# Performance work log

Hardware: AMD Instinct MI355X
Metric: run time of the kernel (lower is better)

Reference implementation:

```python
import jax, jax.numpy as jnp
import numpy as np

N, F, E, T = 50000, 128, 800000, 8


def setup_inputs() -> dict:
    key = jax.random.key(0)
    ks = jax.random.split(key, 10)
    s = 1.0 / np.sqrt(F)
    return {
        "x": jax.random.normal(ks[0], (N, F), jnp.float32),
        "edge_index": jax.random.randint(ks[1], (2, E), 0, N, jnp.int64),
        "edge_weight": jax.random.uniform(ks[2], (E,), jnp.float32),
        "W0": jax.random.normal(ks[3], (F, F), jnp.float32) * s,
        "Wih": jax.random.normal(ks[4], (3 * F, F), jnp.float32) * s,
        "Whh": jax.random.normal(ks[5], (3 * F, F), jnp.float32) * s,
        "bih": jax.random.normal(ks[6], (3 * F,), jnp.float32) * s,
        "bhh": jax.random.normal(ks[7], (3 * F,), jnp.float32) * s,
        "Wlin": jax.random.normal(ks[8], (T, F), jnp.float32) * s,
        "blin": jax.random.normal(ks[9], (T,), jnp.float32) * s,
    }


def _evolve_weight(W0, Wih, Whh, bih, bhh):
    # One GRU step with input = hidden = W0 (rows of weight matrix as batch).
    gi = W0 @ Wih.T + bih  # [F, 3F]
    gh = W0 @ Whh.T + bhh
    ir, iz, inn = jnp.split(gi, 3, axis=1)
    hr, hz, hn = jnp.split(gh, 3, axis=1)
    r = jax.nn.sigmoid(ir + hr)
    z = jax.nn.sigmoid(iz + hz)
    n = jnp.tanh(inn + r * hn)
    return (1.0 - z) * n + z * W0  # [F, F]


def reference(x, edge_index, edge_weight, W0, Wih, Whh, bih, bhh, Wlin, blin):
    n_nodes = x.shape[0]
    W = _evolve_weight(W0, Wih, Whh, bih, bhh)
    # gcn_norm with added self-loops (fill value 1.0), symmetric normalization
    loop = jnp.arange(n_nodes, dtype=edge_index.dtype)
    row = jnp.concatenate([edge_index[0], loop])
    col = jnp.concatenate([edge_index[1], loop])
    ew = jnp.concatenate([edge_weight, jnp.ones((n_nodes,), edge_weight.dtype)])
    deg = jax.ops.segment_sum(ew, col, num_segments=n_nodes)
    dinv = jnp.where(deg > 0, jax.lax.rsqrt(jnp.where(deg > 0, deg, 1.0)), 0.0)
    norm = dinv[row] * ew * dinv[col]  # [E+N]
    xw = x @ W  # [N, F]
    h = jax.ops.segment_sum(norm[:, None] * xw[row], col, num_segments=n_nodes)
    h = jax.nn.relu(h)
    return h @ Wlin.T + blin  # [N, n_target]
```

## Files before the change

kernel.cpp:

```cpp
#include <hip/hip_runtime.h>
#include <math.h>

#define F 128
#define FIX18     262144.0f
#define INV18     (1.0f / 262144.0f)
#define EVB 256

using bf16x8 = __attribute__((ext_vector_type(8))) short;
using f32x4  = __attribute__((ext_vector_type(4))) float;

__device__ inline int read_idx(const int* ei, long long elem, int i64) {
    return i64 ? (int)((const long long*)ei)[elem] : ei[elem];
}
__device__ inline unsigned int f2bf_rn(float f) {
    unsigned int b = __float_as_uint(f);
    return (b + 0x7FFFu + ((b >> 16) & 1u)) >> 16;
}
__device__ inline float bflo(unsigned int u) { return __uint_as_float(u << 16); }
__device__ inline float bfhi(unsigned int u) { return __uint_as_float(u & 0xFFFF0000u); }

__device__ inline void acc8(float* acc, float wt, uint4 v) {
    acc[0] += wt * bflo(v.x); acc[1] += wt * bfhi(v.x);
    acc[2] += wt * bflo(v.y); acc[3] += wt * bfhi(v.y);
    acc[4] += wt * bflo(v.z); acc[5] += wt * bfhi(v.z);
    acc[6] += wt * bflo(v.w); acc[7] += wt * bfhi(v.w);
}

__device__ inline int detect_i64(const int* ei, int* sh) {
    if (threadIdx.x == 0) {
        int i64 = 1;
        for (int j = 0; j < 32; ++j) if (ei[2 * j + 1] != 0) { i64 = 0; break; }
        *sh = i64;
    }
    __syncthreads();
    return *sh;
}

__global__ __launch_bounds__(256) void k_count_evolve(
        const int* __restrict__ ei, const float* __restrict__ ew,
        unsigned int* __restrict__ packed8, int* __restrict__ pos,
        int E, int N,
        const float* __restrict__ W0, const float* __restrict__ Wih,
        const float* __restrict__ Whh, const float* __restrict__ bih,
        const float* __restrict__ bhh,
        unsigned short* __restrict__ Wth, unsigned short* __restrict__ Wtl) {
    __shared__ int i64sh;
    int wave = threadIdx.x >> 6, lane = threadIdx.x & 63;
    if ((int)blockIdx.x >= EVB) {
        int i64 = detect_i64(ei, &i64sh);
        int e = ((int)blockIdx.x - EVB) * 256 + threadIdx.x;
        if (e >= E) return;
        int c = read_idx(ei, (long long)E + e, i64);
        unsigned int copy = blockIdx.x & 7;
        unsigned int u = (1u << 24) | (unsigned int)(ew[e] * FIX18 + 0.5f);
        unsigned int old = atomicAdd(&packed8[(size_t)copy * N + c], u);
        pos[e] = (int)((old >> 24) | (copy << 24));
        return;
    }
    int gw = (int)blockIdx.x * 4 + wave;
    int pairBase = gw * 16;
    int i = pairBase >> 7;
    int jb = pairBase & 127;
    int lp = lane & 15, sl = lane >> 4;
    int j = jb + lp;
    const float* w0p = W0 + (size_t)i * F;
    const float* pir = Wih + (size_t)j * F;
    const float* piz = Wih + (size_t)(j + F) * F;
    const float* pin = Wih + (size_t)(j + 2 * F) * F;
    const float* phr = Whh + (size_t)j * F;
    const float* phz = Whh + (size_t)(j + F) * F;
    const float* phn = Whh + (size_t)(j + 2 * F) * F;
    float air = 0, aiz = 0, ain = 0, ahr = 0, ahz = 0, ahn = 0;
    int k0 = sl * 32;
    #pragma unroll
    for (int kk = 0; kk < 32; kk += 4) {
        int k = k0 + kk;
        float4 w0 = *(const float4*)&w0p[k];
        float4 a;
        a = *(const float4*)&pir[k]; air += w0.x*a.x + w0.y*a.y + w0.z*a.z + w0.w*a.w;
        a = *(const float4*)&piz[k]; aiz += w0.x*a.x + w0.y*a.y + w0.z*a.z + w0.w*a.w;
        a = *(const float4*)&pin[k]; ain += w0.x*a.x + w0.y*a.y + w0.z*a.z + w0.w*a.w;
        a = *(const float4*)&phr[k]; ahr += w0.x*a.x + w0.y*a.y + w0.z*a.z + w0.w*a.w;
        a = *(const float4*)&phz[k]; ahz += w0.x*a.x + w0.y*a.y + w0.z*a.z + w0.w*a.w;
        a = *(const float4*)&phn[k]; ahn += w0.x*a.x + w0.y*a.y + w0.z*a.z + w0.w*a.w;
    }
    air += __shfl_xor(air, 16, 64); air += __shfl_xor(air, 32, 64);
    aiz += __shfl_xor(aiz, 16, 64); aiz += __shfl_xor(aiz, 32, 64);
    ain += __shfl_xor(ain, 16, 64); ain += __shfl_xor(ain, 32, 64);
    ahr += __shfl_xor(ahr, 16, 64); ahr += __shfl_xor(ahr, 32, 64);
    ahz += __shfl_xor(ahz, 16, 64); ahz += __shfl_xor(ahz, 32, 64);
    ahn += __shfl_xor(ahn, 16, 64); ahn += __shfl_xor(ahn, 32, 64);
    if (sl == 0) {
        air += bih[j];          ahr += bhh[j];
        aiz += bih[j + F];      ahz += bhh[j + F];
        ain += bih[j + 2 * F];  ahn += bhh[j + 2 * F];
        float r = 1.0f / (1.0f + expf(-(air + ahr)));
        float z = 1.0f / (1.0f + expf(-(aiz + ahz)));
        float n = tanhf(ain + r * ahn);
        float w = (1.0f - z) * n + z * w0p[j];
        unsigned int hb = f2bf_rn(w);
        float whi = __uint_as_float(hb << 16);
        unsigned int lb = f2bf_rn(w - whi);
        Wth[j * F + i] = (unsigned short)hb;
        Wtl[j * F + i] = (unsigned short)lb;
    }
}

__global__ void k_bsum(const unsigned int* __restrict__ packed8,
                       int* __restrict__ bsum, int N) {
    __shared__ int s[4];
    int i = blockIdx.x * 256 + threadIdx.x;
    int v = 0;
    if (i < N) {
        #pragma unroll
        for (int k = 0; k < 8; ++k)
            v += (int)(packed8[(size_t)k * N + i] >> 24);
    }
    #pragma unroll
    for (int o = 1; o < 64; o <<= 1) v += __shfl_xor(v, o, 64);
    if ((threadIdx.x & 63) == 0) s[threadIdx.x >> 6] = v;
    __syncthreads();
    if (threadIdx.x == 0) bsum[blockIdx.x] = s[0] + s[1] + s[2] + s[3];
}

__global__ void k_offs(const unsigned int* __restrict__ packed8,
                       const int* __restrict__ bsum,
                       int* __restrict__ off, unsigned char* __restrict__ copyBase,
                       float* __restrict__ dinv, int N, int E, int nblk) {
    __shared__ int sdata[256];
    __shared__ int sred[4];
    __shared__ int sbase;
    int t = threadIdx.x;
    int b = blockIdx.x;
    int base = 0;
    for (int s0 = 0; s0 < nblk; s0 += 256) {
        int idx = s0 + t;
        int v = (idx < nblk && idx < b) ? bsum[idx] : 0;
        #pragma unroll
        for (int o = 1; o < 64; o <<= 1) v += __shfl_xor(v, o, 64);
        if ((t & 63) == 0) sred[t >> 6] = v;
        __syncthreads();
        if (t == 0) sbase = sred[0] + sred[1] + sred[2] + sred[3];
        __syncthreads();
        base += sbase;
        __syncthreads();
    }
    int i = b * 256 + t;
    int v = 0;
    unsigned int dsum = 0;
    if (i < N) {
        int run = 0;
        #pragma unroll
        for (int k = 0; k < 8; ++k) {
            unsigned int p = packed8[(size_t)k * N + i];
            copyBase[(size_t)i * 8 + k] = (unsigned char)run;
            run += (int)(p >> 24);
            dsum += (p & 0xFFFFFFu);
        }
        v = run;
    }
    sdata[t] = v;
    __syncthreads();
    #pragma unroll
    for (int s = 1; s < 256; s <<= 1) {
        int add = (t >= s) ? sdata[t - s] : 0;
        __syncthreads();
        sdata[t] += add;
        __syncthreads();
    }
    if (i < N) {
        off[i] = base + sdata[t] - v;
        dinv[i] = rsqrtf(1.0f + (float)dsum * INV18);
        if (i == N - 1) off[N] = E;
    }
}

__global__ __launch_bounds__(256) void k_place_cast(
        const int* __restrict__ ei, const float* __restrict__ ew,
        const int* __restrict__ off, const unsigned char* __restrict__ copyBase,
        const int* __restrict__ pos,
        int2* __restrict__ ep, int E, int placeBlocks,
        const float2* __restrict__ x2, const float* __restrict__ dinv,
        unsigned int* __restrict__ xs, int M) {
    __shared__ int i64sh;
    if ((int)blockIdx.x < placeBlocks) {
        int i64 = detect_i64(ei, &i64sh);
        int e = blockIdx.x * 256 + threadIdx.x;
        if (e >= E) return;
        int r = read_idx(ei, e, i64);
        int c = read_idx(ei, (long long)E + e, i64);
        unsigned int pe = (unsigned int)pos[e];
        int slot = off[c] + (int)copyBase[(size_t)c * 8 + (pe >> 24)] + (int)(pe & 0xFFFFFFu);
        ep[slot] = make_int2(r, __float_as_int(ew[e]));
    } else {
        int id = ((int)blockIdx.x - placeBlocks) * 256 + threadIdx.x;
        if (id >= M) return;
        float di = dinv[id >> 6];
        float2 v = x2[id];
        xs[id] = f2bf_rn(di * v.x) | (f2bf_rn(di * v.y) << 16);
    }
}

__global__ __launch_bounds__(1024) void k_agg_gemm(
        const uint4* __restrict__ xs4, const int* __restrict__ off,
        const int2* __restrict__ ep, const float* __restrict__ dinv,
        const unsigned short* __restrict__ Wth, const unsigned short* __restrict__ Wtl,
        const float* __restrict__ Wlin, const float* __restrict__ blin,
        float* __restrict__ out, int N) {
    __shared__ __align__(16) unsigned int At[64 * 68];
    __shared__ __align__(16) float WlinL[8 * F];
    int t = threadIdx.x;
    int wave = t >> 6, lane = t & 63;
    int row0 = blockIdx.x * 64;
    WlinL[t] = Wlin[t];
    int g = lane >> 4, sl = lane & 15;

    #pragma unroll
    for (int sub = 0; sub < 4; ++sub) {
        int rr = wave * 4 + sub;
        int c = row0 + rr;
        if (c < N) {
            int start = off[c], end = off[c + 1];
            float di = dinv[c];
            float a0[8] = {0,0,0,0,0,0,0,0}, a1[8] = {0,0,0,0,0,0,0,0};
            if (g == 0) {
                uint4 v = xs4[(size_t)c * 16 + sl];
                a0[0] = bflo(v.x); a0[1] = bfhi(v.x);
                a0[2] = bflo(v.y); a0[3] = bfhi(v.y);
                a0[4] = bflo(v.z); a0[5] = bfhi(v.z);
                a0[6] = bflo(v.w); a0[7] = bfhi(v.w);
            }
            int last = end - 1;
            for (int k = start; k < end; k += 16) {
                int iA = k + g, iB = k + g + 4, iC = k + g + 8, iD = k + g + 12;
                int2 eA = ep[min(iA, last)];
                int2 eB = ep[min(iB, last)];
                int2 eC = ep[min(iC, last)];
                int2 eD = ep[min(iD, last)];
                uint4 vA = xs4[(size_t)eA.x * 16 + sl];
                uint4 vB = xs4[(size_t)eB.x * 16 + sl];
                uint4 vC = xs4[(size_t)eC.x * 16 + sl];
                uint4 vD = xs4[(size_t)eD.x * 16 + sl];
                float wA = (iA <= last) ? __int_as_float(eA.y) : 0.f;
                float wB = (iB <= last) ? __int_as_float(eB.y) : 0.f;
                float wC = (iC <= last) ? __int_as_float(eC.y) : 0.f;
                float wD = (iD <= last) ? __int_as_float(eD.y) : 0.f;
                acc8(a0, wA, vA);
                acc8(a1, wB, vB);
                acc8(a0, wC, vC);
                acc8(a1, wD, vD);
            }
            #pragma unroll
            for (int f = 0; f < 8; ++f) {
                float v = a0[f] + a1[f];
                v += __shfl_xor(v, 16, 64);
                v += __shfl_xor(v, 32, 64);
                a0[f] = v;
            }
            if (lane < 16) {
                uint4 o;
                o.x = f2bf_rn(di * a0[0]) | (f2bf_rn(di * a0[1]) << 16);
                o.y = f2bf_rn(di * a0[2]) | (f2bf_rn(di * a0[3]) << 16);
                o.z = f2bf_rn(di * a0[4]) | (f2bf_rn(di * a0[5]) << 16);
                o.w = f2bf_rn(di * a0[6]) | (f2bf_rn(di * a0[7]) << 16);
                *(uint4*)&At[rr * 68 + sl * 4] = o;
            }
        } else if (lane < 16) {
            *(uint4*)&At[rr * 68 + sl * 4] = make_uint4(0u, 0u, 0u, 0u);
        }
    }
    __syncthreads();
    if (wave >= 4) return;

    int q = g;
    const unsigned short* Ash = (const unsigned short*)At;
    int mrow = wave * 16 + sl;
    f32x4 acc[8];
    #pragma unroll
    for (int nt = 0; nt < 8; ++nt) acc[nt] = (f32x4){0.f, 0.f, 0.f, 0.f};
    #pragma unroll
    for (int ko = 0; ko < 4; ++ko) {
        bf16x8 a = *(const bf16x8*)&Ash[mrow * 136 + ko * 32 + q * 8];
        #pragma unroll
        for (int nt = 0; nt < 8; ++nt) {
            int boff = (nt * 16 + sl) * F + ko * 32 + q * 8;
            bf16x8 bh = *(const bf16x8*)&Wth[boff];
            bf16x8 bl = *(const bf16x8*)&Wtl[boff];
            acc[nt] = __builtin_amdgcn_mfma_f32_16x16x32_bf16(a, bh, acc[nt], 0, 0, 0);
            acc[nt] = __builtin_amdgcn_mfma_f32_16x16x32_bf16(a, bl, acc[nt], 0, 0, 0);
        }
    }
    #pragma unroll
    for (int nt = 0; nt < 8; ++nt)
        #pragma unroll
        for (int r = 0; r < 4; ++r) acc[nt][r] = fmaxf(acc[nt][r], 0.f);

    float p[8][4];
    #pragma unroll
    for (int tt = 0; tt < 8; ++tt) {
        float wl[8];
        #pragma unroll
        for (int nt = 0; nt < 8; ++nt) wl[nt] = WlinL[tt * F + nt * 16 + sl];
        #pragma unroll
        for (int r = 0; r < 4; ++r) {
            float s = 0.f;
            #pragma unroll
            for (int nt = 0; nt < 8; ++nt) s += acc[nt][r] * wl[nt];
            p[tt][r] = s;
        }
    }
    #pragma unroll
    for (int tt = 0; tt < 8; ++tt)
        #pragma unroll
        for (int r = 0; r < 4; ++r) {
            float v = p[tt][r];
            v += __shfl_xor(v, 1, 64); v += __shfl_xor(v, 2, 64);
            v += __shfl_xor(v, 4, 64); v += __shfl_xor(v, 8, 64);
            p[tt][r] = v;
        }
    if (sl == 0) {
        #pragma unroll
        for (int r = 0; r < 4; ++r) {
            int row = row0 + wave * 16 + q * 4 + r;
            if (row < N) {
                #pragma unroll
                for (int tt = 0; tt < 8; ++tt)
                    out[(size_t)row * 8 + tt] = p[tt][r] + blin[tt];
            }
        }
    }
}

extern "C" void kernel_launch(void* const* d_in, const int* in_sizes, int n_in,
                              void* d_out, int out_size, void* d_ws, size_t ws_size,
                              hipStream_t stream) {
    const float* x    = (const float*)d_in[0];
    const int*   ei   = (const int*)d_in[1];
    const float* ew   = (const float*)d_in[2];
    const float* W0   = (const float*)d_in[3];
    const float* Wih  = (const float*)d_in[4];
    const float* Whh  = (const float*)d_in[5];
    const float* bih  = (const float*)d_in[6];
    const float* bhh  = (const float*)d_in[7];
    const float* Wlin = (const float*)d_in[8];
    const float* blin = (const float*)d_in[9];
    int N = in_sizes[0] / F;
    int E = in_sizes[1] / 2;
    float* outp = (float*)d_out;

    int nblk = (N + 255) / 256;
    int cntBlocks = (E + 255) / 256;
    int M = N * 64;

    char* wsb = (char*)d_ws;
    size_t cur = 0;
    auto alloc = [&](size_t sz) -> void* {
        void* p = wsb + cur;
        cur = (cur + sz + 255) & ~(size_t)255;
        return p;
    };
    unsigned int* packed8 = (unsigned int*)alloc((size_t)N * 8 * 4);
    float* dinv = (float*)alloc((size_t)N * 4);
    int*   off  = (int*)  alloc((size_t)(N + 1) * 4);
    int*   bsum = (int*)  alloc((size_t)nblk * 4);
    int*   pos  = (int*)  alloc((size_t)E * 4);
    unsigned char* copyBase = (unsigned char*)alloc((size_t)N * 8);
    int2*  ep   = (int2*) alloc((size_t)E * 8);
    unsigned short* Wth = (unsigned short*)alloc((size_t)F * F * 2);
    unsigned short* Wtl = (unsigned short*)alloc((size_t)F * F * 2);
    unsigned int* xs    = (unsigned int*)alloc((size_t)N * 64 * 4);
    (void)ws_size; (void)n_in; (void)out_size;

    hipMemsetAsync(packed8, 0, (size_t)N * 8 * 4, stream);
    hipLaunchKernelGGL(k_count_evolve, dim3(EVB + cntBlocks), dim3(256), 0, stream,
                       ei, ew, packed8, pos, E, N,
                       W0, Wih, Whh, bih, bhh, Wth, Wtl);
    hipLaunchKernelGGL(k_bsum, dim3(nblk), dim3(256), 0, stream, packed8, bsum, N);
    hipLaunchKernelGGL(k_offs, dim3(nblk), dim3(256), 0, stream,
                       packed8, bsum, off, copyBase, dinv, N, E, nblk);
    hipLaunchKernelGGL(k_place_cast, dim3(cntBlocks + (M + 255) / 256), dim3(256), 0, stream,
                       ei, ew, off, copyBase, pos, ep, E, cntBlocks,
                       (const float2*)x, dinv, xs, M);
    hipLaunchKernelGGL(k_agg_gemm, dim3((N + 63) / 64), dim3(1024), 0, stream,
                       (const uint4*)xs, off, ep, dinv, Wth, Wtl, Wlin, blin, outp, N);
}
```

Before: 216.7 us.

## Split fused aggregation+GEMM kernel into separate aggregation and GEMM kernels

The fused kernel, in which 1024-thread blocks did the gather aggregation and then only 4 of 16 waves ran the MFMA GEMM, is split in two. A 256-thread aggregation kernel (one wave per node) writes bf16 aggregated rows to a new global buffer, and a 256-thread GEMM kernel loads 64 rows into LDS and runs the MFMA plus the output projection. This removes the block-wide barrier that tied aggregation load imbalance to GEMM idle waves and raises scheduling flexibility. In exchange it adds an extra kernel launch and a round trip of about 12.8 MB of intermediate data through global memory.

Result: no change. 212.5 us (-1.9%).

```diff
diff --git a/kernel.cpp b/kernel.cpp
--- a/kernel.cpp
+++ b/kernel.cpp
@@ -201,80 +201,88 @@
     }
 }
 
-__global__ __launch_bounds__(1024) void k_agg_gemm(
-        const uint4* __restrict__ xs4, const int* __restrict__ off,
-        const int2* __restrict__ ep, const float* __restrict__ dinv,
-        const unsigned short* __restrict__ Wth, const unsigned short* __restrict__ Wtl,
-        const float* __restrict__ Wlin, const float* __restrict__ blin,
-        float* __restrict__ out, int N) {
+__global__ __launch_bounds__(256) void k_agg2(const uint4* __restrict__ xs4,
+                                              const int* __restrict__ off,
+                                              const int2* __restrict__ ep,
+                                              const float* __restrict__ dinv,
+                                              uint4* __restrict__ hagg4, int N) {
+    int wave = threadIdx.x >> 6, lane = threadIdx.x & 63;
+    int c = blockIdx.x * 4 + wave;
+    if (c >= N) return;
+    int g = lane >> 4, sl = lane & 15;
+    int start = off[c], end = off[c + 1];
+    float di = dinv[c];
+    float a0[8] = {0,0,0,0,0,0,0,0}, a1[8] = {0,0,0,0,0,0,0,0};
+    if (g == 0) {
+        uint4 v = xs4[(size_t)c * 16 + sl];
+        a0[0] = bflo(v.x); a0[1] = bfhi(v.x);
+        a0[2] = bflo(v.y); a0[3] = bfhi(v.y);
+        a0[4] = bflo(v.z); a0[5] = bfhi(v.z);
+        a0[6] = bflo(v.w); a0[7] = bfhi(v.w);
+    }
+    int last = end - 1;
+    for (int k = start; k < end; k += 16) {
+        int iA = k + g, iB = k + g + 4, iC = k + g + 8, iD = k + g + 12;
+        int2 eA = ep[min(iA, last)];
+        int2 eB = ep[min(iB, last)];
+        int2 eC = ep[min(iC, last)];
+        int2 eD = ep[min(iD, last)];
+        uint4 vA = xs4[(size_t)eA.x * 16 + sl];
+        uint4 vB = xs4[(size_t)eB.x * 16 + sl];
+        uint4 vC = xs4[(size_t)eC.x * 16 + sl];
+        uint4 vD = xs4[(size_t)eD.x * 16 + sl];
+        float wA = (iA <= last) ? __int_as_float(eA.y) : 0.f;
+        float wB = (iB <= last) ? __int_as_float(eB.y) : 0.f;
+        float wC = (iC <= last) ? __int_as_float(eC.y) : 0.f;
+        float wD = (iD <= last) ? __int_as_float(eD.y) : 0.f;
+        acc8(a0, wA, vA);
+        acc8(a1, wB, vB);
+        acc8(a0, wC, vC);
+        acc8(a1, wD, vD);
+    }
+    #pragma unroll
+    for (int f = 0; f < 8; ++f) {
+        float v = a0[f] + a1[f];
+        v += __shfl_xor(v, 16, 64);
+        v += __shfl_xor(v, 32, 64);
+        a0[f] = v;
+    }
+    if (lane < 16) {
+        uint4 o;
+        o.x = f2bf_rn(di * a0[0]) | (f2bf_rn(di * a0[1]) << 16);
+        o.y = f2bf_rn(di * a0[2]) | (f2bf_rn(di * a0[3]) << 16);
+        o.z = f2bf_rn(di * a0[4]) | (f2bf_rn(di * a0[5]) << 16);
+        o.w = f2bf_rn(di * a0[6]) | (f2bf_rn(di * a0[7]) << 16);
+        hagg4[(size_t)c * 16 + lane] = o;
+    }
+}
+
+__global__ __launch_bounds__(256) void k_gemm(const uint4* __restrict__ hagg4,
+                                              const unsigned short* __restrict__ Wth,
+                                              const unsigned short* __restrict__ Wtl,
+                                              const float* __restrict__ Wlin,
+                                              const float* __restrict__ blin,
+                                              float* __restrict__ out, int N) {
     __shared__ __align__(16) unsigned int At[64 * 68];
     __shared__ __align__(16) float WlinL[8 * F];
     int t = threadIdx.x;
+    int row0 = blockIdx.x * 64;
+    #pragma unroll
+    for (int it = 0; it < 4; ++it) {
+        int idx = it * 256 + t;
+        int rr = idx >> 4, c4 = idx & 15;
+        uint4 v = make_uint4(0u, 0u, 0u, 0u);
+        if (row0 + rr < N) v = hagg4[(size_t)(row0 + rr) * 16 + c4];
+        *(uint4*)&At[rr * 68 + c4 * 4] = v;
+    }
+    *(float4*)&WlinL[t * 4] = *(const float4*)&Wlin[t * 4];
+    __syncthreads();
+
     int wave = t >> 6, lane = t & 63;
-    int row0 = blockIdx.x * 64;
-    WlinL[t] = Wlin[t];
-    int g = lane >> 4, sl = lane & 15;
-
-    #pragma unroll
-    for (int sub = 0; sub < 4; ++sub) {
-        int rr = wave * 4 + sub;
-        int c = row0 + rr;
-        if (c < N) {
-            int start = off[c], end = off[c + 1];
-            float di = dinv[c];
-            float a0[8] = {0,0,0,0,0,0,0,0}, a1[8] = {0,0,0,0,0,0,0,0};
-            if (g == 0) {
-                uint4 v = xs4[(size_t)c * 16 + sl];
-                a0[0] = bflo(v.x); a0[1] = bfhi(v.x);
-                a0[2] = bflo(v.y); a0[3] = bfhi(v.y);
-                a0[4] = bflo(v.z); a0[5] = bfhi(v.z);
-                a0[6] = bflo(v.w); a0[7] = bfhi(v.w);
-            }
-            int last = end - 1;
-            for (int k = start; k < end; k += 16) {
-                int iA = k + g, iB = k + g + 4, iC = k + g + 8, iD = k + g + 12;
-                int2 eA = ep[min(iA, last)];
-                int2 eB = ep[min(iB, last)];
-                int2 eC = ep[min(iC, last)];
-                int2 eD = ep[min(iD, last)];
-                uint4 vA = xs4[(size_t)eA.x * 16 + sl];
-                uint4 vB = xs4[(size_t)eB.x * 16 + sl];
-                uint4 vC = xs4[(size_t)eC.x * 16 + sl];
-                uint4 vD = xs4[(size_t)eD.x * 16 + sl];
-                float wA = (iA <= last) ? __int_as_float(eA.y) : 0.f;
-                float wB = (iB <= last) ? __int_as_float(eB.y) : 0.f;
-                float wC = (iC <= last) ? __int_as_float(eC.y) : 0.f;
-                float wD = (iD <= last) ? __int_as_float(eD.y) : 0.f;
-                acc8(a0, wA, vA);
-                acc8(a1, wB, vB);
-                acc8(a0, wC, vC);
-                acc8(a1, wD, vD);
-            }
-            #pragma unroll
-            for (int f = 0; f < 8; ++f) {
-                float v = a0[f] + a1[f];
-                v += __shfl_xor(v, 16, 64);
-                v += __shfl_xor(v, 32, 64);
-                a0[f] = v;
-            }
-            if (lane < 16) {
-                uint4 o;
-                o.x = f2bf_rn(di * a0[0]) | (f2bf_rn(di * a0[1]) << 16);
-                o.y = f2bf_rn(di * a0[2]) | (f2bf_rn(di * a0[3]) << 16);
-                o.z = f2bf_rn(di * a0[4]) | (f2bf_rn(di * a0[5]) << 16);
-                o.w = f2bf_rn(di * a0[6]) | (f2bf_rn(di * a0[7]) << 16);
-                *(uint4*)&At[rr * 68 + sl * 4] = o;
-            }
-        } else if (lane < 16) {
-            *(uint4*)&At[rr * 68 + sl * 4] = make_uint4(0u, 0u, 0u, 0u);
-        }
-    }
-    __syncthreads();
-    if (wave >= 4) return;
-
-    int q = g;
+    int sl = lane & 15, q = lane >> 4;
     const unsigned short* Ash = (const unsigned short*)At;
     int mrow = wave * 16 + sl;
+
     f32x4 acc[8];
     #pragma unroll
     for (int nt = 0; nt < 8; ++nt) acc[nt] = (f32x4){0.f, 0.f, 0.f, 0.f};
@@ -369,6 +377,7 @@
     unsigned short* Wth = (unsigned short*)alloc((size_t)F * F * 2);
     unsigned short* Wtl = (unsigned short*)alloc((size_t)F * F * 2);
     unsigned int* xs    = (unsigned int*)alloc((size_t)N * 64 * 4);
+    unsigned int* hagg  = (unsigned int*)alloc((size_t)N * 64 * 4);
     (void)ws_size; (void)n_in; (void)out_size;
 
     hipMemsetAsync(packed8, 0, (size_t)N * 8 * 4, stream);
@@ -381,6 +390,8 @@
     hipLaunchKernelGGL(k_place_cast, dim3(cntBlocks + (M + 255) / 256), dim3(256), 0, stream,
                        ei, ew, off, copyBase, pos, ep, E, cntBlocks,
                        (const float2*)x, dinv, xs, M);
-    hipLaunchKernelGGL(k_agg_gemm, dim3((N + 63) / 64), dim3(1024), 0, stream,
-                       (const uint4*)xs, off, ep, dinv, Wth, Wtl, Wlin, blin, outp, N);
-}
+    hipLaunchKernelGGL(k_agg2, dim3((N + 3) / 4), dim3(256), 0, stream,
+                       (const uint4*)xs, off, ep, dinv, (uint4*)hagg, N);
+    hipLaunchKernelGGL(k_gemm, dim3((N + 63) / 64), dim3(256), 0, stream,
+                       (const uint4*)hagg, Wth, Wtl, Wlin, blin, outp, N);
+}
```
